# Kernel tuning notes

Measured on AMD Instinct MI355X. Metric: run time of the kernel, lower is better.

The kernel has to match this reference:

```python
import jax, jax.numpy as jnp
import numpy as np

B, LQ, LK = 4, 2048, 2048
DQ, DC = 1024, 1024
H, DH = 16, 64
INNER = H * DH
LN_EPS = 1e-5
TAU_INIT = DH ** -0.5


def layernorm(x, w, b):
    mu = jnp.mean(x, axis=-1, keepdims=True)
    var = jnp.var(x, axis=-1, keepdims=True)
    return (x - mu) * jax.lax.rsqrt(var + LN_EPS) * w + b


def l2norm(x, eps=1e-12):
    # matches F.normalize(dim=-1): x / max(||x||, eps)
    n = jnp.sqrt(jnp.sum(x * x, axis=-1, keepdims=True))
    return x / jnp.maximum(n, eps)


def setup_inputs() -> dict:
    key = jax.random.key(0)
    ks = jax.random.split(key, 8)
    s = lambda d: (1.0 / np.sqrt(d)).astype(np.float32) if isinstance(d, np.ndarray) else np.float32(1.0 / np.sqrt(d))
    return {
        "x": jax.random.normal(ks[0], (B, LQ, DQ), jnp.float32),
        "context": jax.random.normal(ks[1], (B, LK, DC), jnp.float32),
        "key_padding_mask": jax.random.bernoulli(ks[2], 0.1, (B, LK)),
        "ln_q_w": jnp.ones((DQ,), jnp.float32),
        "ln_q_b": jnp.zeros((DQ,), jnp.float32),
        "ln_ctx_w": jnp.ones((DC,), jnp.float32),
        "ln_ctx_b": jnp.zeros((DC,), jnp.float32),
        "Wq": jax.random.normal(ks[3], (DQ, INNER), jnp.float32) * s(DQ),
        "Wk": jax.random.normal(ks[4], (DC, INNER), jnp.float32) * s(DC),
        "Wv": jax.random.normal(ks[5], (DC, INNER), jnp.float32) * s(DC),
        "Wo": jax.random.normal(ks[6], (INNER, DQ), jnp.float32) * s(INNER),
        "tau": jnp.float32(TAU_INIT),
    }


def reference(x, context, key_padding_mask, ln_q_w, ln_q_b, ln_ctx_w, ln_ctx_b, Wq, Wk, Wv, Wo, tau):
    q_in = layernorm(x, ln_q_w, ln_q_b)
    kv_in = layernorm(context, ln_ctx_w, ln_ctx_b)
    q = (q_in @ Wq).reshape(B, LQ, H, DH)   # [B,Lq,H,Dh]
    k = (kv_in @ Wk).reshape(B, LK, H, DH)
    v = (kv_in @ Wv).reshape(B, LK, H, DH)
    q = l2norm(q)
    k = l2norm(k)
    scores = jnp.einsum('bqhd,bkhd->bhqk', q, k) / (tau + 1e-6)
    scores = jnp.where(key_padding_mask[:, None, None, :], -jnp.inf, scores)
    attn = jax.nn.softmax(scores, axis=-1)
    out = jnp.einsum('bhqk,bkhd->bqhd', attn, v).reshape(B, LQ, INNER)
    return out @ Wo
```

## Files before the change

kernel.cpp:

```cpp
#include <hip/hip_runtime.h>

typedef unsigned short u16;
typedef __bf16 bf16x8 __attribute__((ext_vector_type(8)));
typedef short s16x4 __attribute__((ext_vector_type(4)));
typedef float f32x4 __attribute__((ext_vector_type(4)));

__device__ __forceinline__ u16 f2bf(float f) {
  unsigned u = __float_as_uint(f);
  unsigned r = u + 0x7fffu + ((u >> 16) & 1u);
  return (u16)(r >> 16);
}

__device__ __forceinline__ unsigned cvt_pk(float a, float b) {
  unsigned r;
  asm("v_cvt_pk_bf16_f32 %0, %1, %2" : "=v"(r) : "v"(a), "v"(b));
  return r;
}

#if __has_builtin(__builtin_amdgcn_exp2f)
#define EXP2(x) __builtin_amdgcn_exp2f(x)
#else
#define EXP2(x) exp2f(x)
#endif

__device__ __forceinline__ void async_cp16(const void* g, void* l) {
  __builtin_amdgcn_global_load_lds((__attribute__((address_space(1))) void*)g,
                                   (__attribute__((address_space(3))) void*)l,
                                   16, 0, 0);
}

#define MFMA32(a, b, c) __builtin_amdgcn_mfma_f32_16x16x32_bf16(a, b, c, 0, 0, 0)

#if __has_builtin(__builtin_amdgcn_mfma_f32_16x16x16bf16_1k)
#define MFMA16(a, b, c) __builtin_amdgcn_mfma_f32_16x16x16bf16_1k(a, b, c, 0, 0, 0)
#else
__device__ __forceinline__ f32x4 mfma16_fb(s16x4 a, s16x4 b, f32x4 c) {
  asm("v_mfma_f32_16x16x16_bf16 %0, %1, %2, %0" : "+v"(c) : "v"(a), "v"(b));
  return c;
}
#define MFMA16(a, b, c) mfma16_fb(a, b, c)
#endif

__global__ __launch_bounds__(256)
void ln_cast2(const float* __restrict__ X0, const float* __restrict__ X1,
              const float* __restrict__ W0, const float* __restrict__ B0,
              const float* __restrict__ W1, const float* __restrict__ B1,
              u16* __restrict__ Y0, u16* __restrict__ Y1) {
  __shared__ float red[8];
  const int blk = blockIdx.x, t = threadIdx.x;
  const int sel = blk >> 13;
  const int row = blk & 8191;
  const float* X = sel ? X1 : X0;
  const float* W = sel ? W1 : W0;
  const float* Bv = sel ? B1 : B0;
  u16* Y = sel ? Y1 : Y0;
  const int wave = t >> 6, lane = t & 63;
  const float4 v = ((const float4*)(X + (size_t)row * 1024))[t];
  float s  = v.x + v.y + v.z + v.w;
  float ss = v.x*v.x + v.y*v.y + v.z*v.z + v.w*v.w;
#pragma unroll
  for (int m = 32; m; m >>= 1) { s += __shfl_xor(s, m, 64); ss += __shfl_xor(ss, m, 64); }
  if (lane == 0) { red[wave] = s; red[4 + wave] = ss; }
  __syncthreads();
  float S  = red[0] + red[1] + red[2] + red[3];
  float SS = red[4] + red[5] + red[6] + red[7];
  float mu  = S * (1.0f / 1024.0f);
  float var = SS * (1.0f / 1024.0f) - mu * mu;
  float rstd = rsqrtf(var + 1e-5f);
  const float4 wv = ((const float4*)W)[t];
  const float4 bv = ((const float4*)Bv)[t];
  ushort4 o;
  o.x = f2bf((v.x - mu) * rstd * wv.x + bv.x);
  o.y = f2bf((v.y - mu) * rstd * wv.y + bv.y);
  o.z = f2bf((v.z - mu) * rstd * wv.z + bv.z);
  o.w = f2bf((v.w - mu) * rstd * wv.w + bv.w);
  ((ushort4*)(Y + (size_t)row * 1024))[t] = o;
}

__global__ __launch_bounds__(256)
void wtrans4(const float* __restrict__ Wq, const float* __restrict__ Wk,
             const float* __restrict__ Wv, const float* __restrict__ Wo,
             u16* __restrict__ WqT, u16* __restrict__ WkT,
             u16* __restrict__ WvT, u16* __restrict__ WoT) {
  __shared__ float t[64][65];
  const int z = blockIdx.z;
  const float* W = z == 0 ? Wq : (z == 1 ? Wk : (z == 2 ? Wv : Wo));
  u16* WT = z == 0 ? WqT : (z == 1 ? WkT : (z == 2 ? WvT : WoT));
  const int k0 = blockIdx.y * 64, n0 = blockIdx.x * 64;
  const int lr = threadIdx.x >> 4, lc = threadIdx.x & 15;
#pragma unroll
  for (int r = 0; r < 4; ++r) {
    int row = r * 16 + lr;
    float4 v = *(const float4*)(W + (size_t)(k0 + row) * 1024 + n0 + lc * 4);
    t[row][lc*4+0] = v.x; t[row][lc*4+1] = v.y; t[row][lc*4+2] = v.z; t[row][lc*4+3] = v.w;
  }
  __syncthreads();
#pragma unroll
  for (int r = 0; r < 4; ++r) {
    int n = r * 16 + lr;
    ushort4 o;
    o.x = f2bf(t[lc*4+0][n]); o.y = f2bf(t[lc*4+1][n]);
    o.z = f2bf(t[lc*4+2][n]); o.w = f2bf(t[lc*4+3][n]);
    *(ushort4*)(WT + (size_t)(n0 + n) * 1024 + k0 + lc * 4) = o;
  }
}

__global__ __launch_bounds__(256)
void vtrans(const float* __restrict__ V, u16* __restrict__ VT) {
  __shared__ float t[64][65];
  const int b = blockIdx.z, h = blockIdx.y, kk0 = blockIdx.x * 64;
  const int lr = threadIdx.x >> 4, lc = threadIdx.x & 15;
#pragma unroll
  for (int r = 0; r < 4; ++r) {
    int row = r * 16 + lr;
    float4 v = *(const float4*)(V + (size_t)(b * 2048 + kk0 + row) * 1024 + h * 64 + lc * 4);
    t[row][lc*4+0] = v.x; t[row][lc*4+1] = v.y; t[row][lc*4+2] = v.z; t[row][lc*4+3] = v.w;
  }
  __syncthreads();
#pragma unroll
  for (int r = 0; r < 4; ++r) {
    int d = r * 16 + lr;
    ushort4 o;
    o.x = f2bf(t[lc*4+0][d]); o.y = f2bf(t[lc*4+1][d]);
    o.z = f2bf(t[lc*4+2][d]); o.w = f2bf(t[lc*4+3][d]);
    *(ushort4*)(VT + ((size_t)(b * 16 + h) * 64 + d) * 2048 + kk0 + lc * 4) = o;
  }
}

__global__ __launch_bounds__(256, 2)
void gemm_qkv(const u16* __restrict__ qin, const u16* __restrict__ kvin,
              const u16* __restrict__ WqT, const u16* __restrict__ WkT,
              const u16* __restrict__ WvT,
              u16* __restrict__ qbf, u16* __restrict__ kbf,
              float* __restrict__ vscr, const float* __restrict__ taup) {
  __shared__ __align__(16) u16 As[128 * 64];
  __shared__ __align__(16) u16 Bs[128 * 64];
  const int z = blockIdx.z;
  const u16* A  = z == 0 ? qin : kvin;
  const u16* Bt = z == 0 ? WqT : (z == 1 ? WkT : WvT);
  const int tid = threadIdx.x;
  const int wave = tid >> 6, lane = tid & 63;
  const int quad = lane >> 4, l15 = lane & 15;
  const int m0 = blockIdx.y * 128, n0 = blockIdx.x * 128;
  const int wm = (wave >> 1) * 64, wn = (wave & 1) * 64;
  const int srow = lane >> 3, scol = (lane & 7) * 8;
  const int K = 1024, N = 1024;

  const f32x4 fz = {0.f, 0.f, 0.f, 0.f};
  f32x4 acc[4][4];
#pragma unroll
  for (int i = 0; i < 4; ++i)
#pragma unroll
    for (int j = 0; j < 4; ++j) acc[i][j] = fz;

  for (int kt = 0; kt < K; kt += 64) {
    __syncthreads();
#pragma unroll
    for (int r = 0; r < 4; ++r) {
      const int c = r * 4 + wave;
      const int row = c * 8 + srow;
      async_cp16(A  + (size_t)(m0 + row) * K + kt + scol, (char*)As + c * 1024);
      async_cp16(Bt + (size_t)(n0 + row) * K + kt + scol, (char*)Bs + c * 1024);
    }
    __syncthreads();
#pragma unroll
    for (int ks = 0; ks < 2; ++ks) {
      bf16x8 af[4], bfr[4];
#pragma unroll
      for (int i = 0; i < 4; ++i)
        af[i] = *(const bf16x8*)(const void*)(As + (wm + i * 16 + l15) * 64 + ks * 32 + quad * 8);
#pragma unroll
      for (int j = 0; j < 4; ++j)
        bfr[j] = *(const bf16x8*)(const void*)(Bs + (wn + j * 16 + l15) * 64 + ks * 32 + quad * 8);
#pragma unroll
      for (int i = 0; i < 4; ++i)
#pragma unroll
        for (int j = 0; j < 4; ++j)
          acc[i][j] = MFMA32(af[i], bfr[j], acc[i][j]);
    }
  }

  if (z < 2) {
    const float tsc = z == 0 ? 1.44269504f / (taup[0] + 1e-6f) : 1.0f;
    u16* Y = z == 0 ? qbf : kbf;
#pragma unroll
    for (int i = 0; i < 4; ++i)
#pragma unroll
      for (int e = 0; e < 4; ++e) {
        float ss = 0.f;
#pragma unroll
        for (int j = 0; j < 4; ++j) ss = fmaf(acc[i][j][e], acc[i][j][e], ss);
        ss += __shfl_xor(ss, 1, 64); ss += __shfl_xor(ss, 2, 64);
        ss += __shfl_xor(ss, 4, 64); ss += __shfl_xor(ss, 8, 64);
        float sc = tsc / fmaxf(sqrtf(ss), 1e-12f);
        int row = m0 + wm + i * 16 + quad * 4 + e;
#pragma unroll
        for (int j = 0; j < 4; ++j)
          Y[(size_t)row * N + n0 + wn + j * 16 + l15] = f2bf(acc[i][j][e] * sc);
      }
  } else {
#pragma unroll
    for (int i = 0; i < 4; ++i)
#pragma unroll
      for (int j = 0; j < 4; ++j)
#pragma unroll
        for (int e = 0; e < 4; ++e) {
          int row = m0 + wm + i * 16 + quad * 4 + e;
          int col = n0 + wn + j * 16 + l15;
          vscr[(size_t)row * N + col] = acc[i][j][e];
        }
  }
}

__global__ __launch_bounds__(256, 2)
void gemm_bt(const u16* __restrict__ A, const u16* __restrict__ Bt,
             float* __restrict__ C, int M, int N, int K) {
  __shared__ __align__(16) u16 As[128 * 64];
  __shared__ __align__(16) u16 Bs[128 * 64];
  const int tid = threadIdx.x;
  const int wave = tid >> 6, lane = tid & 63;
  const int quad = lane >> 4, l15 = lane & 15;
  const int m0 = blockIdx.y * 128, n0 = blockIdx.x * 128;
  const int wm = (wave >> 1) * 64, wn = (wave & 1) * 64;
  const int srow = lane >> 3, scol = (lane & 7) * 8;

  const f32x4 fz = {0.f, 0.f, 0.f, 0.f};
  f32x4 acc[4][4];
#pragma unroll
  for (int i = 0; i < 4; ++i)
#pragma unroll
    for (int j = 0; j < 4; ++j) acc[i][j] = fz;

  for (int kt = 0; kt < K; kt += 64) {
    __syncthreads();
#pragma unroll
    for (int r = 0; r < 4; ++r) {
      const int c = r * 4 + wave;
      const int row = c * 8 + srow;
      async_cp16(A  + (size_t)(m0 + row) * K + kt + scol, (char*)As + c * 1024);
      async_cp16(Bt + (size_t)(n0 + row) * K + kt + scol, (char*)Bs + c * 1024);
    }
    __syncthreads();
#pragma unroll
    for (int ks = 0; ks < 2; ++ks) {
      bf16x8 af[4], bfr[4];
#pragma unroll
      for (int i = 0; i < 4; ++i)
        af[i] = *(const bf16x8*)(const void*)(As + (wm + i * 16 + l15) * 64 + ks * 32 + quad * 8);
#pragma unroll
      for (int j = 0; j < 4; ++j)
        bfr[j] = *(const bf16x8*)(const void*)(Bs + (wn + j * 16 + l15) * 64 + ks * 32 + quad * 8);
#pragma unroll
      for (int i = 0; i < 4; ++i)
#pragma unroll
        for (int j = 0; j < 4; ++j)
          acc[i][j] = MFMA32(af[i], bfr[j], acc[i][j]);
    }
  }
#pragma unroll
  for (int i = 0; i < 4; ++i)
#pragma unroll
    for (int j = 0; j < 4; ++j)
#pragma unroll
      for (int e = 0; e < 4; ++e) {
        int row = m0 + wm + i * 16 + quad * 4 + e;
        int col = n0 + wn + j * 16 + l15;
        C[(size_t)row * N + col] = acc[i][j][e];
      }
}

__global__ __launch_bounds__(256, 2)
void flash_attn9(const u16* __restrict__ Qb, const u16* __restrict__ Kb,
                 const u16* __restrict__ Vt, const int* __restrict__ mask,
                 u16* __restrict__ Ob) {
  __shared__ __align__(16) u16 QPs[256 * 64];
  __shared__ __align__(16) u16 Ks[2][64 * 64];
  __shared__ __align__(16) u16 Vs[2][64 * 64];
  __shared__ __align__(16) float Msf[2048];
  const int tid = threadIdx.x, w = tid >> 6, lane = tid & 63;
  const int quad = lane >> 4, l15 = lane & 15;
  const int b = blockIdx.z, h = blockIdx.y, q0 = blockIdx.x * 256;
  const int srow = lane >> 3;
  const int scolX = ((lane & 7) ^ srow) * 8;
  const int fsw = ((l15 & 7) << 4);

#pragma unroll
  for (int r = 0; r < 8; ++r) {
    int c = w * 8 + r;
    async_cp16(Qb + (size_t)(b * 2048 + q0 + c * 8 + srow) * 1024 + h * 64 + scolX,
               (char*)QPs + c * 1024);
  }
#pragma unroll
  for (int r = 0; r < 2; ++r) {
    int c = w * 2 + r;
    async_cp16(Kb + (size_t)(b * 2048 + c * 8 + srow) * 1024 + h * 64 + scolX,
               (char*)Ks[0] + c * 1024);
    async_cp16(Vt + ((size_t)(b * 16 + h) * 64 + c * 8 + srow) * 2048 + scolX,
               (char*)Vs[0] + c * 1024);
  }
  {
    const int* mp = mask + b * 2048 + tid * 8;
    int4 ma = *(const int4*)mp;
    int4 mb = *(const int4*)(mp + 4);
    float4 o0, o1;
    o0.x = ma.x ? -3.0e38f : 0.f; o0.y = ma.y ? -3.0e38f : 0.f;
    o0.z = ma.z ? -3.0e38f : 0.f; o0.w = ma.w ? -3.0e38f : 0.f;
    o1.x = mb.x ? -3.0e38f : 0.f; o1.y = mb.y ? -3.0e38f : 0.f;
    o1.z = mb.z ? -3.0e38f : 0.f; o1.w = mb.w ? -3.0e38f : 0.f;
    *(float4*)(Msf + tid * 8)     = o0;
    *(float4*)(Msf + tid * 8 + 4) = o1;
  }
  __syncthreads();

  bf16x8 aq[4][2];
#pragma unroll
  for (int i = 0; i < 4; ++i)
#pragma unroll
    for (int ks = 0; ks < 2; ++ks)
      aq[i][ks] = *(const bf16x8*)(const void*)(
          (const char*)QPs + (w * 64 + i * 16 + l15) * 128 + (((ks * 4 + quad) << 4) ^ fsw));

  const f32x4 fz = {0.f, 0.f, 0.f, 0.f};
  f32x4 o[4][4];
  float rs[4] = {0.f, 0.f, 0.f, 0.f};
#pragma unroll
  for (int dt = 0; dt < 4; ++dt)
#pragma unroll
    for (int i = 0; i < 4; ++i) o[dt][i] = fz;

  int cur = 0;
  for (int kt = 0; kt < 2048; kt += 64) {
    if (kt + 64 < 2048) {
#pragma unroll
      for (int r = 0; r < 2; ++r) {
        int c = w * 2 + r;
        async_cp16(Kb + (size_t)(b * 2048 + kt + 64 + c * 8 + srow) * 1024 + h * 64 + scolX,
                   (char*)Ks[cur ^ 1] + c * 1024);
        async_cp16(Vt + ((size_t)(b * 16 + h) * 64 + c * 8 + srow) * 2048 + kt + 64 + scolX,
                   (char*)Vs[cur ^ 1] + c * 1024);
      }
    }

    bf16x8 kb[4][2];
#pragma unroll
    for (int kkt = 0; kkt < 4; ++kkt)
#pragma unroll
      for (int ks = 0; ks < 2; ++ks)
        kb[kkt][ks] = *(const bf16x8*)(const void*)(
            (const char*)Ks[cur] + (kkt * 16 + l15) * 128 + (((ks * 4 + quad) << 4) ^ fsw));

#pragma unroll
    for (int kkt = 0; kkt < 4; ++kkt) {
      f32x4 bias = *(const f32x4*)(Msf + kt + kkt * 16 + quad * 4);

      s16x4 pf[4];
#pragma unroll
      for (int i = 0; i < 4; ++i) {
        f32x4 st = MFMA32(kb[kkt][0], aq[i][0], bias);
        st = MFMA32(kb[kkt][1], aq[i][1], st);
        float p0 = EXP2(st[0]), p1 = EXP2(st[1]);
        float p2 = EXP2(st[2]), p3 = EXP2(st[3]);
        rs[i] += (p0 + p1) + (p2 + p3);
        union { unsigned u[2]; s16x4 s; } pk;
        pk.u[0] = cvt_pk(p0, p1);
        pk.u[1] = cvt_pk(p2, p3);
        pf[i] = pk.s;
      }
      __builtin_amdgcn_s_setprio(1);
#pragma unroll
      for (int dt = 0; dt < 4; ++dt) {
        s16x4 va = *(const s16x4*)(const void*)(
            (const char*)Vs[cur] + (dt * 16 + l15) * 128 + ((kkt * 32 + quad * 8) ^ fsw));
#pragma unroll
        for (int i = 0; i < 4; ++i)
          o[dt][i] = MFMA16(va, pf[i], o[dt][i]);
      }
      __builtin_amdgcn_s_setprio(0);
    }
    __syncthreads();
    cur ^= 1;
  }

  float inv[4];
#pragma unroll
  for (int i = 0; i < 4; ++i) {
    float v = rs[i];
    v += __shfl_xor(v, 16, 64);
    v += __shfl_xor(v, 32, 64);
    inv[i] = 1.0f / v;
  }

  u16* strip = QPs + w * 64 * 64;
#pragma unroll
  for (int dt = 0; dt < 4; ++dt)
#pragma unroll
    for (int i = 0; i < 4; ++i) {
      union { unsigned u[2]; s16x4 s; } pk;
      pk.u[0] = cvt_pk(o[dt][i][0] * inv[i], o[dt][i][1] * inv[i]);
      pk.u[1] = cvt_pk(o[dt][i][2] * inv[i], o[dt][i][3] * inv[i]);
      *(s16x4*)(void*)((char*)strip + (i * 16 + l15) * 128 + ((dt * 32 + quad * 8) ^ fsw)) = pk.s;
    }
#pragma unroll
  for (int pass = 0; pass < 8; ++pass) {
    int row = pass * 8 + (lane >> 3), oct = lane & 7;
    int4 v = *(const int4*)(const void*)((const char*)strip + row * 128 + ((oct ^ (row & 7)) << 4));
    *(int4*)(Ob + (size_t)(b * 2048 + q0 + w * 64 + row) * 1024 + h * 64 + oct * 8) = v;
  }
}

extern "C" void kernel_launch(void* const* d_in, const int* in_sizes, int n_in,
                              void* d_out, int out_size, void* d_ws, size_t ws_size,
                              hipStream_t stream) {
  const float* x    = (const float*)d_in[0];
  const float* ctx  = (const float*)d_in[1];
  const int*   mask = (const int*)d_in[2];
  const float* lnqw = (const float*)d_in[3];
  const float* lnqb = (const float*)d_in[4];
  const float* lncw = (const float*)d_in[5];
  const float* lncb = (const float*)d_in[6];
  const float* Wq   = (const float*)d_in[7];
  const float* Wk   = (const float*)d_in[8];
  const float* Wv   = (const float*)d_in[9];
  const float* Wo   = (const float*)d_in[10];
  const float* tau  = (const float*)d_in[11];
  float* out = (float*)d_out;
  char* ws = (char*)d_ws;
  const size_t MB = 1024 * 1024;

  u16* qin  = (u16*)(ws + 0 * MB);
  u16* kvin = (u16*)(ws + 16 * MB);
  u16* WqT  = (u16*)(ws + 32 * MB);
  u16* WkT  = (u16*)(ws + 34 * MB);
  u16* WvT  = (u16*)(ws + 36 * MB);
  u16* WoT  = (u16*)(ws + 38 * MB);
  u16* qbf  = (u16*)(ws + 40 * MB);
  u16* kbf  = (u16*)(ws + 56 * MB);
  u16* vT   = (u16*)(ws + 72 * MB);
  float* scr = out;
  u16* attn = qin;

  ln_cast2<<<16384, 256, 0, stream>>>(x, ctx, lnqw, lnqb, lncw, lncb, qin, kvin);
  wtrans4<<<dim3(16, 16, 4), 256, 0, stream>>>(Wq, Wk, Wv, Wo, WqT, WkT, WvT, WoT);

  gemm_qkv<<<dim3(8, 64, 3), 256, 0, stream>>>(qin, kvin, WqT, WkT, WvT,
                                               qbf, kbf, scr, tau);

  vtrans<<<dim3(32, 16, 4), 256, 0, stream>>>(scr, vT);

  flash_attn9<<<dim3(8, 16, 4), 256, 0, stream>>>(qbf, kbf, vT, mask, attn);

  gemm_bt<<<dim3(8, 64), 256, 0, stream>>>(attn, WoT, out, 8192, 1024, 1024);
}
```

Measured before the change: 340.8 us.

## Halve flash-attention query tile and alias Q staging with K/V buffers

The attention kernel now processes 128 query rows per block (32 per wave) instead of 256, doubling the grid to 1024 blocks. Q staging shares one LDS array with the K/V double buffers and the output strip, which cuts shared memory use and the register accumulators per thread. This should improve occupancy and load balance across CUs, but each K/V tile is now reused by half as many queries, so K/V global and LDS traffic per query doubles. Extra barriers are added at startup.

```diff
diff --git a/kernel.cpp b/kernel.cpp
--- a/kernel.cpp
+++ b/kernel.cpp
@@ -270,33 +270,23 @@
 }
 
 __global__ __launch_bounds__(256, 2)
-void flash_attn9(const u16* __restrict__ Qb, const u16* __restrict__ Kb,
-                 const u16* __restrict__ Vt, const int* __restrict__ mask,
-                 u16* __restrict__ Ob) {
-  __shared__ __align__(16) u16 QPs[256 * 64];
-  __shared__ __align__(16) u16 Ks[2][64 * 64];
-  __shared__ __align__(16) u16 Vs[2][64 * 64];
+void flash_attn10(const u16* __restrict__ Qb, const u16* __restrict__ Kb,
+                  const u16* __restrict__ Vt, const int* __restrict__ mask,
+                  u16* __restrict__ Ob) {
+  __shared__ __align__(16) u16 SH[16384];
   __shared__ __align__(16) float Msf[2048];
   const int tid = threadIdx.x, w = tid >> 6, lane = tid & 63;
   const int quad = lane >> 4, l15 = lane & 15;
-  const int b = blockIdx.z, h = blockIdx.y, q0 = blockIdx.x * 256;
+  const int b = blockIdx.z, h = blockIdx.y, q0 = blockIdx.x * 128;
   const int srow = lane >> 3;
   const int scolX = ((lane & 7) ^ srow) * 8;
   const int fsw = ((l15 & 7) << 4);
 
 #pragma unroll
-  for (int r = 0; r < 8; ++r) {
-    int c = w * 8 + r;
+  for (int r = 0; r < 4; ++r) {
+    int c = w * 4 + r;
     async_cp16(Qb + (size_t)(b * 2048 + q0 + c * 8 + srow) * 1024 + h * 64 + scolX,
-               (char*)QPs + c * 1024);
-  }
-#pragma unroll
-  for (int r = 0; r < 2; ++r) {
-    int c = w * 2 + r;
-    async_cp16(Kb + (size_t)(b * 2048 + c * 8 + srow) * 1024 + h * 64 + scolX,
-               (char*)Ks[0] + c * 1024);
-    async_cp16(Vt + ((size_t)(b * 16 + h) * 64 + c * 8 + srow) * 2048 + scolX,
-               (char*)Vs[0] + c * 1024);
+               (char*)SH + c * 1024);
   }
   {
     const int* mp = mask + b * 2048 + tid * 8;
@@ -312,32 +302,47 @@
   }
   __syncthreads();
 
-  bf16x8 aq[4][2];
-#pragma unroll
-  for (int i = 0; i < 4; ++i)
+  bf16x8 aq[2][2];
+#pragma unroll
+  for (int i = 0; i < 2; ++i)
 #pragma unroll
     for (int ks = 0; ks < 2; ++ks)
       aq[i][ks] = *(const bf16x8*)(const void*)(
-          (const char*)QPs + (w * 64 + i * 16 + l15) * 128 + (((ks * 4 + quad) << 4) ^ fsw));
+          (const char*)SH + (w * 32 + i * 16 + l15) * 128 + (((ks * 4 + quad) << 4) ^ fsw));
+  __syncthreads();
+
+#pragma unroll
+  for (int r = 0; r < 2; ++r) {
+    int c = w * 2 + r;
+    async_cp16(Kb + (size_t)(b * 2048 + c * 8 + srow) * 1024 + h * 64 + scolX,
+               (char*)SH + c * 1024);
+    async_cp16(Vt + ((size_t)(b * 16 + h) * 64 + c * 8 + srow) * 2048 + scolX,
+               (char*)SH + 16384 + c * 1024);
+  }
+  __syncthreads();
 
   const f32x4 fz = {0.f, 0.f, 0.f, 0.f};
-  f32x4 o[4][4];
-  float rs[4] = {0.f, 0.f, 0.f, 0.f};
+  f32x4 o[4][2];
+  float rs[2] = {0.f, 0.f};
 #pragma unroll
   for (int dt = 0; dt < 4; ++dt)
 #pragma unroll
-    for (int i = 0; i < 4; ++i) o[dt][i] = fz;
+    for (int i = 0; i < 2; ++i) o[dt][i] = fz;
 
   int cur = 0;
   for (int kt = 0; kt < 2048; kt += 64) {
+    const char* Kc = (const char*)SH + cur * 8192;
+    const char* Vc = (const char*)SH + 16384 + cur * 8192;
     if (kt + 64 < 2048) {
+      char* Kn = (char*)SH + (cur ^ 1) * 8192;
+      char* Vn = (char*)SH + 16384 + (cur ^ 1) * 8192;
 #pragma unroll
       for (int r = 0; r < 2; ++r) {
         int c = w * 2 + r;
         async_cp16(Kb + (size_t)(b * 2048 + kt + 64 + c * 8 + srow) * 1024 + h * 64 + scolX,
-                   (char*)Ks[cur ^ 1] + c * 1024);
+                   Kn + c * 1024);
         async_cp16(Vt + ((size_t)(b * 16 + h) * 64 + c * 8 + srow) * 2048 + kt + 64 + scolX,
-                   (char*)Vs[cur ^ 1] + c * 1024);
+                   Vn + c * 1024);
       }
     }
 
@@ -347,15 +352,15 @@
 #pragma unroll
       for (int ks = 0; ks < 2; ++ks)
         kb[kkt][ks] = *(const bf16x8*)(const void*)(
-            (const char*)Ks[cur] + (kkt * 16 + l15) * 128 + (((ks * 4 + quad) << 4) ^ fsw));
+            Kc + (kkt * 16 + l15) * 128 + (((ks * 4 + quad) << 4) ^ fsw));
 
 #pragma unroll
     for (int kkt = 0; kkt < 4; ++kkt) {
       f32x4 bias = *(const f32x4*)(Msf + kt + kkt * 16 + quad * 4);
 
-      s16x4 pf[4];
-#pragma unroll
-      for (int i = 0; i < 4; ++i) {
+      s16x4 pf[2];
+#pragma unroll
+      for (int i = 0; i < 2; ++i) {
         f32x4 st = MFMA32(kb[kkt][0], aq[i][0], bias);
         st = MFMA32(kb[kkt][1], aq[i][1], st);
         float p0 = EXP2(st[0]), p1 = EXP2(st[1]);
@@ -370,9 +375,9 @@
 #pragma unroll
       for (int dt = 0; dt < 4; ++dt) {
         s16x4 va = *(const s16x4*)(const void*)(
-            (const char*)Vs[cur] + (dt * 16 + l15) * 128 + ((kkt * 32 + quad * 8) ^ fsw));
-#pragma unroll
-        for (int i = 0; i < 4; ++i)
+            Vc + (dt * 16 + l15) * 128 + ((kkt * 32 + quad * 8) ^ fsw));
+#pragma unroll
+        for (int i = 0; i < 2; ++i)
           o[dt][i] = MFMA16(va, pf[i], o[dt][i]);
       }
       __builtin_amdgcn_s_setprio(0);
@@ -381,30 +386,30 @@
     cur ^= 1;
   }
 
-  float inv[4];
-#pragma unroll
-  for (int i = 0; i < 4; ++i) {
+  float inv[2];
+#pragma unroll
+  for (int i = 0; i < 2; ++i) {
     float v = rs[i];
     v += __shfl_xor(v, 16, 64);
     v += __shfl_xor(v, 32, 64);
     inv[i] = 1.0f / v;
   }
 
-  u16* strip = QPs + w * 64 * 64;
+  u16* strip = SH + w * 2048;
 #pragma unroll
   for (int dt = 0; dt < 4; ++dt)
 #pragma unroll
-    for (int i = 0; i < 4; ++i) {
+    for (int i = 0; i < 2; ++i) {
       union { unsigned u[2]; s16x4 s; } pk;
       pk.u[0] = cvt_pk(o[dt][i][0] * inv[i], o[dt][i][1] * inv[i]);
       pk.u[1] = cvt_pk(o[dt][i][2] * inv[i], o[dt][i][3] * inv[i]);
       *(s16x4*)(void*)((char*)strip + (i * 16 + l15) * 128 + ((dt * 32 + quad * 8) ^ fsw)) = pk.s;
     }
 #pragma unroll
-  for (int pass = 0; pass < 8; ++pass) {
+  for (int pass = 0; pass < 4; ++pass) {
     int row = pass * 8 + (lane >> 3), oct = lane & 7;
     int4 v = *(const int4*)(const void*)((const char*)strip + row * 128 + ((oct ^ (row & 7)) << 4));
-    *(int4*)(Ob + (size_t)(b * 2048 + q0 + w * 64 + row) * 1024 + h * 64 + oct * 8) = v;
+    *(int4*)(Ob + (size_t)(b * 2048 + q0 + w * 32 + row) * 1024 + h * 64 + oct * 8) = v;
   }
 }
 
@@ -447,7 +452,7 @@
 
   vtrans<<<dim3(32, 16, 4), 256, 0, stream>>>(scr, vT);
 
-  flash_attn9<<<dim3(8, 16, 4), 256, 0, stream>>>(qbf, kbf, vT, mask, attn);
+  flash_attn10<<<dim3(16, 16, 4), 256, 0, stream>>>(qbf, kbf, vT, mask, attn);
 
   gemm_bt<<<dim3(8, 64), 256, 0, stream>>>(attn, WoT, out, 8192, 1024, 1024);
 }
```

Measured after the change: 335.3 us. Within noise of the previous version (-1.6%).
